# Optimization experiments

Hardware: AMD Instinct MI355X
Metric: run time of the kernel (lower is better)

## Reference

```python
import jax, jax.numpy as jnp
import numpy as np
import math

D_MODEL = 1024
NHEAD = 16
D_K = D_MODEL // NHEAD
B = 4
S = 2048


def setup_inputs() -> dict:
    key = jax.random.key(0)
    ks = jax.random.split(key, 12)
    scale = 1.0 / math.sqrt(D_MODEL)
    inp = {
        "query": jax.random.normal(ks[0], (B, S, D_MODEL), dtype=jnp.float32),
        "key": jax.random.normal(ks[1], (B, S, D_MODEL), dtype=jnp.float32),
        "value": jax.random.normal(ks[2], (B, S, D_MODEL), dtype=jnp.float32),
        "mask": jnp.ones((B, 1, 1, S), dtype=jnp.int32),
        "Wq": jax.random.normal(ks[3], (D_MODEL, D_MODEL), dtype=jnp.float32) * scale,
        "bq": jax.random.normal(ks[4], (D_MODEL,), dtype=jnp.float32) * scale,
        "Wk": jax.random.normal(ks[5], (D_MODEL, D_MODEL), dtype=jnp.float32) * scale,
        "bk": jax.random.normal(ks[6], (D_MODEL,), dtype=jnp.float32) * scale,
        "Wv": jax.random.normal(ks[7], (D_MODEL, D_MODEL), dtype=jnp.float32) * scale,
        "bv": jax.random.normal(ks[8], (D_MODEL,), dtype=jnp.float32) * scale,
        "Wo": jax.random.normal(ks[9], (D_MODEL, D_MODEL), dtype=jnp.float32) * scale,
        "bo": jax.random.normal(ks[10], (D_MODEL,), dtype=jnp.float32) * scale,
    }
    return inp


def reference(query, key, value, mask, Wq, bq, Wk, bk, Wv, bv, Wo, bo):
    b, s, _ = query.shape
    # torch nn.Linear: y = x @ W.T + b ; weights stored [out, in]
    def proj(x, W, bias):
        y = jnp.einsum("bsd,ed->bse", x, W) + bias
        return y.reshape(b, s, NHEAD, D_K).transpose(0, 2, 1, 3)  # [b,h,s,dk]

    Q = proj(query, Wq, bq)
    K = proj(key, Wk, bk)
    V = proj(value, Wv, bv)

    scores = jnp.einsum("bhqd,bhkd->bhqk", Q, K) / math.sqrt(D_K)  # [b,h,s,s]
    scores = jnp.where(mask == 0, jnp.float32(-1e9), scores)
    attn = jax.nn.softmax(scores, axis=-1)
    # dropout p=0.0 (eval): identity
    context = jnp.einsum("bhqk,bhkd->bhqd", attn, V)
    context = context.transpose(0, 2, 1, 3).reshape(b, s, D_MODEL)
    out = jnp.einsum("bsd,ed->bse", context, Wo) + bo
    return out
```

## Files before the change

### kernel.cpp

```cpp
#include <hip/hip_runtime.h>

typedef unsigned short u16;
typedef unsigned int u32;
typedef _Float16 f16;
typedef __attribute__((ext_vector_type(8))) _Float16 f16x8;
typedef __attribute__((ext_vector_type(4))) float f32x4;
typedef __attribute__((ext_vector_type(16))) float f32x16;
typedef __attribute__((ext_vector_type(8))) short short8;
typedef __attribute__((ext_vector_type(4))) short short4v;
typedef __attribute__((ext_vector_type(2))) u32 u32x2;

#define DM 1024
#define NB 4
#define SS 2048
#define NH 16
#define DK 64
#define MROWS (NB * SS)
#define QSCALE 0.1803368801111244f

__device__ __forceinline__ u16 f2h(float x) {
    return __builtin_bit_cast(u16, (f16)x);
}
__device__ __forceinline__ u32 pkh(float lo, float hi) {
    return __builtin_bit_cast(u32, __builtin_amdgcn_cvt_pkrtz(lo, hi));
}

__device__ __forceinline__ f32x4 mfma16h(f16x8 a, f16x8 b, f32x4 c) {
    return __builtin_amdgcn_mfma_f32_16x16x32_f16(a, b, c, 0, 0, 0);
}
__device__ __forceinline__ f32x16 mfma32h(f16x8 a, f16x8 b, f32x16 c) {
    return __builtin_amdgcn_mfma_f32_32x32x16_f16(a, b, c, 0, 0, 0);
}

__device__ __forceinline__ void gload16(const void* g, void* l) {
    __builtin_amdgcn_global_load_lds(
        (const __attribute__((address_space(1))) void*)g,
        (__attribute__((address_space(3))) void*)l, 16, 0, 0);
}

#define PLSWAP(a, b) asm volatile("v_permlane32_swap_b32 %0, %1" : "+v"(a), "+v"(b))


__global__ __launch_bounds__(256) void prep_k(
    const float* __restrict__ q, const float* __restrict__ k, const float* __restrict__ v,
    const float* __restrict__ wq, const float* __restrict__ wk, const float* __restrict__ wv,
    const float* __restrict__ wo,
    u16* __restrict__ xq, u16* __restrict__ xk, u16* __restrict__ xv,
    u16* __restrict__ wqb, u16* __restrict__ wkb, u16* __restrict__ wvb,
    u16* __restrict__ wob) {
    const int NX8 = 1 << 20, NW8 = 1 << 17;
    int i = blockIdx.x * 256 + threadIdx.x;
    const float* src;
    u16* dst;
    int j;
    if (i < 3 * NX8) {
        const int which = i >> 20;
        j = i & (NX8 - 1);
        src = (which == 0) ? q : (which == 1) ? k : v;
        dst = (which == 0) ? xq : (which == 1) ? xk : xv;
    } else {
        const int i2 = i - 3 * NX8;
        const int which = i2 >> 17;
        j = i2 & (NW8 - 1);
        src = (which == 0) ? wq : (which == 1) ? wk : (which == 2) ? wv : wo;
        dst = (which == 0) ? wqb : (which == 1) ? wkb : (which == 2) ? wvb : wob;
    }
    const f32x4* p = (const f32x4*)src + (size_t)j * 2;
    f32x4 a = p[0], b = p[1];
    short8 r;
#pragma unroll
    for (int e = 0; e < 8; e++) r[e] = (short)f2h((e < 4) ? a[e] : b[e - 4]);
    *((short8*)dst + j) = r;
}


__global__ __launch_bounds__(256) void qkv_gemm(
    const u16* __restrict__ Xq, const u16* __restrict__ Xk, const u16* __restrict__ Xv,
    const u16* __restrict__ Wq, const u16* __restrict__ Wk, const u16* __restrict__ Wv,
    const float* __restrict__ bq, const float* __restrict__ bk, const float* __restrict__ bv,
    u16* __restrict__ Qb, u16* __restrict__ Kb, u16* __restrict__ Vb) {
    __shared__ u16 As[128 * 32];
    __shared__ u16 Bs[128 * 32];
    __shared__ u16 Tt[32 * 136];
    const int which = blockIdx.y >> 3;
    const int col0 = (blockIdx.y & 7) * 128;
    const u16* A = (which == 0) ? Xq : (which == 1) ? Xk : Xv;
    const u16* Bw = (which == 0) ? Wq : (which == 1) ? Wk : Wv;
    const float* bias = (which == 0) ? bq : (which == 1) ? bk : bv;
    const float oscale = (which == 0) ? QSCALE : 1.0f;

    const int tid = threadIdx.x;
    const int wid = tid >> 6, lane = tid & 63;
    const int row0 = blockIdx.x * 128;
    const int wr = wid >> 1, wc = wid & 1;
    const int l15 = lane & 15, l4 = lane >> 4;
    const int K = DM;

    f32x4 acc[4][4];
#pragma unroll
    for (int i = 0; i < 4; i++)
#pragma unroll
        for (int j = 0; j < 4; j++) acc[i][j] = f32x4{0.f, 0.f, 0.f, 0.f};

    const int srow = wid * 32 + (lane >> 2);
    const int scol = (lane & 3) * 8;
    const u16* Ag = A + (size_t)(row0 + srow) * K + scol;
    const u16* Bg = Bw + (size_t)(col0 + srow) * K + scol;
    u16* ldsA0 = &As[wid * 1024];
    u16* ldsB0 = &Bs[wid * 1024];

    for (int kt = 0; kt < 32; ++kt) {
        const int ko = kt * 32;
        gload16(Ag + ko, ldsA0);
        gload16(Ag + (size_t)16 * K + ko, ldsA0 + 512);
        gload16(Bg + ko, ldsB0);
        gload16(Bg + (size_t)16 * K + ko, ldsB0 + 512);
        __syncthreads();

        f16x8 af[4], bfr[4];
#pragma unroll
        for (int i = 0; i < 4; i++)
            af[i] = *(const f16x8*)&As[(wr * 64 + i * 16 + l15) * 32 + l4 * 8];
#pragma unroll
        for (int i = 0; i < 4; i++)
            bfr[i] = *(const f16x8*)&Bs[(wc * 64 + i * 16 + l15) * 32 + l4 * 8];
#pragma unroll
        for (int i = 0; i < 4; i++)
#pragma unroll
            for (int j = 0; j < 4; j++) acc[i][j] = mfma16h(af[i], bfr[j], acc[i][j]);
        __syncthreads();
    }

    if (which == 2) {
        const int b = row0 >> 11;
        const int s0 = row0 & (SS - 1);
#pragma unroll
        for (int c = 0; c < 4; ++c) {
            if ((c >> 1) == wc) {
#pragma unroll
                for (int jj = 0; jj < 2; ++jj) {
                    const int j = (c & 1) * 2 + jj;
                    const int col = col0 + wc * 64 + j * 16 + l15;
                    const float bv2 = bias[col];
                    const int dkl = jj * 16 + l15;
#pragma unroll
                    for (int i = 0; i < 4; ++i) {
                        const int sl = wr * 64 + i * 16 + l4 * 4;
                        u32 lo = pkh(acc[i][j][0] + bv2, acc[i][j][1] + bv2);
                        u32 hi2 = pkh(acc[i][j][2] + bv2, acc[i][j][3] + bv2);
                        *(u32x2*)&Tt[dkl * 136 + sl] = u32x2{lo, hi2};
                    }
                }
            }
            __syncthreads();
            {
                const int row = tid >> 3;
                const int col = col0 + c * 32 + row;
                const int h = col >> 6, dk = col & (DK - 1);
                const size_t vbase = ((size_t)(b * NH + h) * DK + dk) * SS + s0;
#pragma unroll
                for (int u = 0; u < 2; ++u) {
                    const int ch = (tid & 7) * 2 + u;
                    f32x4 dat = *(const f32x4*)&Tt[row * 136 + ch * 8];
                    *(f32x4*)&Vb[vbase + ch * 8] = dat;
                }
            }
            __syncthreads();
        }
        return;
    }

    u16* outp = (which == 0) ? Qb : Kb;
#pragma unroll
    for (int j = 0; j < 4; j++) {
        const int col = col0 + wc * 64 + j * 16 + l15;
        const float bv2 = bias[col];
        const int h = col >> 6, dk = col & (DK - 1);
#pragma unroll
        for (int i = 0; i < 4; i++) {
            const int rowb = row0 + wr * 64 + i * 16 + l4 * 4;
#pragma unroll
            for (int r = 0; r < 4; r++) {
                const float v = (acc[i][j][r] + bv2) * oscale;
                const int row = rowb + r;
                const int b = row >> 11, s = row & (SS - 1);
                outp[((size_t)(b * NH + h) * SS + s) * DK + dk] = f2h(v);
            }
        }
    }
}


__global__ __launch_bounds__(256) void out_gemm(const u16* __restrict__ A,
                                                const u16* __restrict__ Bw,
                                                const float* __restrict__ bias,
                                                float* __restrict__ C) {
    __shared__ u16 As[128 * 32];
    __shared__ u16 Bs[128 * 32];
    const int tid = threadIdx.x;
    const int wid = tid >> 6, lane = tid & 63;
    const int row0 = blockIdx.x * 128, col0 = blockIdx.y * 128;
    const int wr = wid >> 1, wc = wid & 1;
    const int l15 = lane & 15, l4 = lane >> 4;
    const int K = DM, N = DM;

    f32x4 acc[4][4];
#pragma unroll
    for (int i = 0; i < 4; i++)
#pragma unroll
        for (int j = 0; j < 4; j++) acc[i][j] = f32x4{0.f, 0.f, 0.f, 0.f};

    const int srow = wid * 32 + (lane >> 2);
    const int scol = (lane & 3) * 8;
    const u16* Ag = A + (size_t)(row0 + srow) * K + scol;
    const u16* Bg = Bw + (size_t)(col0 + srow) * K + scol;
    u16* ldsA0 = &As[wid * 1024];
    u16* ldsB0 = &Bs[wid * 1024];

    for (int kt = 0; kt < 32; ++kt) {
        const int ko = kt * 32;
        gload16(Ag + ko, ldsA0);
        gload16(Ag + (size_t)16 * K + ko, ldsA0 + 512);
        gload16(Bg + ko, ldsB0);
        gload16(Bg + (size_t)16 * K + ko, ldsB0 + 512);
        __syncthreads();

        f16x8 af[4], bfr[4];
#pragma unroll
        for (int i = 0; i < 4; i++)
            af[i] = *(const f16x8*)&As[(wr * 64 + i * 16 + l15) * 32 + l4 * 8];
#pragma unroll
        for (int i = 0; i < 4; i++)
            bfr[i] = *(const f16x8*)&Bs[(wc * 64 + i * 16 + l15) * 32 + l4 * 8];
#pragma unroll
        for (int i = 0; i < 4; i++)
#pragma unroll
            for (int j = 0; j < 4; j++) acc[i][j] = mfma16h(af[i], bfr[j], acc[i][j]);
        __syncthreads();
    }

#pragma unroll
    for (int j = 0; j < 4; j++) {
        const int col = col0 + wc * 64 + j * 16 + l15;
        const float bv = bias[col];
#pragma unroll
        for (int i = 0; i < 4; i++) {
            const int rowb = row0 + wr * 64 + i * 16 + l4 * 4;
#pragma unroll
            for (int r = 0; r < 4; r++)
                C[(size_t)(rowb + r) * N + col] = acc[i][j][r] + bv;
        }
    }
}


__global__ __launch_bounds__(256, 2) void attn6_k(const u16* __restrict__ Q,
                                                  const u16* __restrict__ Kp,
                                                  const u16* __restrict__ Vt,
                                                  u16* __restrict__ ctx) {
    __shared__ u16 Ks[2][4096];
    __shared__ u16 Vs[2][4096];
    const int tid = threadIdx.x, wid = tid >> 6, lane = tid & 63;
    const int l31 = lane & 31, hi = lane >> 5;

    const int flat = blockIdx.y * gridDim.x + blockIdx.x;
    const int xcd = flat & 7, idx = flat >> 3;
    const int bh = xcd * 8 + (idx & 7);
    const int q0 = (idx >> 3) * 256 + wid * 64;

    const size_t base = (size_t)bh * SS * DK;

    f16x8 qf0[4], qf1[4];
#pragma unroll
    for (int dch = 0; dch < 4; dch++) {
        qf0[dch] = *(const f16x8*)&Q[base + (size_t)(q0 + l31) * DK + dch * 16 + hi * 8];
        qf1[dch] = *(const f16x8*)&Q[base + (size_t)(q0 + 32 + l31) * DK + dch * 16 + hi * 8];
    }

    f32x16 acc00, acc01, acc10, acc11;
#pragma unroll
    for (int r = 0; r < 16; r++) { acc00[r] = 0.f; acc01[r] = 0.f; acc10[r] = 0.f; acc11[r] = 0.f; }
    float lrow0 = 0.f, lrow1 = 0.f;

    const int srowA = wid * 16 + (lane >> 3);
    const int srowB = srowA + 8;
    const int scolb = (lane & 7) * 16;
    const int swA = (scolb ^ ((srowA & 7) << 4)) >> 1;
    const int swB = (scolb ^ ((srowB & 7) << 4)) >> 1;
    const u16* KgA = Kp + base + (size_t)srowA * DK + swA;
    const u16* KgB = Kp + base + (size_t)srowB * DK + swB;
    const u16* VgA = Vt + ((size_t)bh * DK + srowA) * SS + swA;
    const u16* VgB = Vt + ((size_t)bh * DK + srowB) * SS + swB;
    const int dstA = wid * 1024, dstB = wid * 1024 + 512;

    gload16(KgA, &Ks[0][dstA]);
    gload16(KgB, &Ks[0][dstB]);
    gload16(VgA, &Vs[0][dstA]);
    gload16(VgB, &Vs[0][dstB]);
    const u16 *KgAn = KgA + 64 * DK, *KgBn = KgB + 64 * DK;
    const u16 *VgAn = VgA + 64, *VgBn = VgB + 64;

    int roff[2][4];
#pragma unroll
    for (int t = 0; t < 2; t++)
#pragma unroll
        for (int c = 0; c < 4; c++)
            roff[t][c] = (t * 32 + l31) * 128 + ((c * 32 + hi * 16) ^ ((l31 & 7) << 4));

#define ATT_BODY(CUR, KT)                                                              \
    {                                                                                  \
        __syncthreads();                                                               \
        if ((KT) + 1 < 32) {                                                           \
            gload16(KgAn, &Ks[(CUR) ^ 1][dstA]);                                       \
            gload16(KgBn, &Ks[(CUR) ^ 1][dstB]);                                       \
            gload16(VgAn, &Vs[(CUR) ^ 1][dstA]);                                       \
            gload16(VgBn, &Vs[(CUR) ^ 1][dstB]);                                       \
            KgAn += 64 * DK; KgBn += 64 * DK;                                          \
            VgAn += 64; VgBn += 64;                                                    \
        }                                                                              \
        const char* kb = (const char*)&Ks[CUR][0];                                     \
        f16x8 kf0[4], kf1[4];                                                          \
        _Pragma("unroll") for (int d = 0; d < 4; d++) {                                \
            kf0[d] = *(const f16x8*)(kb + roff[0][d]);                                 \
            kf1[d] = *(const f16x8*)(kb + roff[1][d]);                                 \
        }                                                                              \
        f32x16 st00 = {}, st01 = {}, st10 = {}, st11 = {};                             \
        __builtin_amdgcn_s_setprio(1);                                                 \
        _Pragma("unroll") for (int d = 0; d < 4; d++) {                                \
            st00 = mfma32h(kf0[d], qf0[d], st00);                                      \
            st01 = mfma32h(kf1[d], qf0[d], st01);                                      \
            st10 = mfma32h(kf0[d], qf1[d], st10);                                      \
            st11 = mfma32h(kf1[d], qf1[d], st11);                                      \
        }                                                                              \
        __builtin_amdgcn_s_setprio(0);                                                 \
        _Pragma("unroll") for (int r = 0; r < 16; r++) {                               \
            st00[r] = __builtin_amdgcn_exp2f(st00[r]);                                 \
            st01[r] = __builtin_amdgcn_exp2f(st01[r]);                                 \
            st10[r] = __builtin_amdgcn_exp2f(st10[r]);                                 \
            st11[r] = __builtin_amdgcn_exp2f(st11[r]);                                 \
        }                                                                              \
        {                                                                              \
            f32x16 t0 = st00 + st01, t1 = st10 + st11;                                 \
            _Pragma("unroll") for (int s2 = 8; s2 >= 1; s2 >>= 1)                      \
                _Pragma("unroll") for (int r = 0; r < s2; r++) {                       \
                    t0[r] += t0[r + s2];                                               \
                    t1[r] += t1[r + s2];                                               \
                }                                                                      \
            lrow0 += t0[0] + __shfl_xor(t0[0], 32);                                    \
            lrow1 += t1[0] + __shfl_xor(t1[0], 32);                                    \
        }                                                                              \
        u32 a0[8], a1[8], b0[8], b1[8];                                                \
        _Pragma("unroll") for (int j = 0; j < 8; j++) {                                \
            a0[j] = pkh(st00[2 * j], st00[2 * j + 1]);                                 \
            a1[j] = pkh(st01[2 * j], st01[2 * j + 1]);                                 \
            b0[j] = pkh(st10[2 * j], st10[2 * j + 1]);                                 \
            b1[j] = pkh(st11[2 * j], st11[2 * j + 1]);                                 \
        }                                                                              \
        PLSWAP(a0[0], a0[2]); PLSWAP(a0[1], a0[3]);                                    \
        PLSWAP(a0[4], a0[6]); PLSWAP(a0[5], a0[7]);                                    \
        PLSWAP(a1[0], a1[2]); PLSWAP(a1[1], a1[3]);                                    \
        PLSWAP(a1[4], a1[6]); PLSWAP(a1[5], a1[7]);                                    \
        PLSWAP(b0[0], b0[2]); PLSWAP(b0[1], b0[3]);                                    \
        PLSWAP(b0[4], b0[6]); PLSWAP(b0[5], b0[7]);                                    \
        PLSWAP(b1[0], b1[2]); PLSWAP(b1[1], b1[3]);                                    \
        PLSWAP(b1[4], b1[6]); PLSWAP(b1[5], b1[7]);                                    \
        union PU { u32 u[4]; f16x8 v; };                                               \
        PU q00, q01, q02, q03, q10, q11, q12, q13;                                     \
        q00.u[0] = a0[0]; q00.u[1] = a0[1]; q00.u[2] = a0[2]; q00.u[3] = a0[3];        \
        q01.u[0] = a0[4]; q01.u[1] = a0[5]; q01.u[2] = a0[6]; q01.u[3] = a0[7];        \
        q02.u[0] = a1[0]; q02.u[1] = a1[1]; q02.u[2] = a1[2]; q02.u[3] = a1[3];        \
        q03.u[0] = a1[4]; q03.u[1] = a1[5]; q03.u[2] = a1[6]; q03.u[3] = a1[7];        \
        q10.u[0] = b0[0]; q10.u[1] = b0[1]; q10.u[2] = b0[2]; q10.u[3] = b0[3];        \
        q11.u[0] = b0[4]; q11.u[1] = b0[5]; q11.u[2] = b0[6]; q11.u[3] = b0[7];        \
        q12.u[0] = b1[0]; q12.u[1] = b1[1]; q12.u[2] = b1[2]; q12.u[3] = b1[3];        \
        q13.u[0] = b1[4]; q13.u[1] = b1[5]; q13.u[2] = b1[6]; q13.u[3] = b1[7];        \
        f16x8 pb0[4] = {q00.v, q01.v, q02.v, q03.v};                                   \
        f16x8 pb1[4] = {q10.v, q11.v, q12.v, q13.v};                                   \
        const char* vb = (const char*)&Vs[CUR][0];                                     \
        f16x8 va0[4], va1[4];                                                          \
        _Pragma("unroll") for (int ks = 0; ks < 4; ks++) {                             \
            va0[ks] = *(const f16x8*)(vb + roff[0][ks]);                               \
            va1[ks] = *(const f16x8*)(vb + roff[1][ks]);                               \
        }                                                                              \
        __builtin_amdgcn_s_setprio(1);                                                 \
        _Pragma("unroll") for (int ks = 0; ks < 4; ks++) {                             \
            acc00 = mfma32h(va0[ks], pb0[ks], acc00);                                  \
            acc01 = mfma32h(va1[ks], pb0[ks], acc01);                                  \
            acc10 = mfma32h(va0[ks], pb1[ks], acc10);                                  \
            acc11 = mfma32h(va1[ks], pb1[ks], acc11);                                  \
        }                                                                              \
        __builtin_amdgcn_s_setprio(0);                                                 \
    }

    for (int kt = 0; kt < 32; kt += 2) {
        ATT_BODY(0, kt);
        ATT_BODY(1, kt + 1);
    }
#undef ATT_BODY

    const int b = bh >> 4, h = bh & (NH - 1);
    const float inv0 = 1.f / lrow0;
    const float inv1 = 1.f / lrow1;
    {
        const int s = q0 + l31;
        const size_t ro = ((size_t)b * SS + s) * DM + h * DK;
#pragma unroll
        for (int g = 0; g < 4; g++) {
            short4v vh;
#pragma unroll
            for (int e = 0; e < 4; e++) vh[e] = (short)f2h(acc00[g * 4 + e] * inv0);
            *(short4v*)&ctx[ro + hi * 4 + g * 8] = vh;
#pragma unroll
            for (int e = 0; e < 4; e++) vh[e] = (short)f2h(acc01[g * 4 + e] * inv0);
            *(short4v*)&ctx[ro + 32 + hi * 4 + g * 8] = vh;
        }
    }
    {
        const int s = q0 + 32 + l31;
        const size_t ro = ((size_t)b * SS + s) * DM + h * DK;
#pragma unroll
        for (int g = 0; g < 4; g++) {
            short4v vh;
#pragma unroll
            for (int e = 0; e < 4; e++) vh[e] = (short)f2h(acc10[g * 4 + e] * inv1);
            *(short4v*)&ctx[ro + hi * 4 + g * 8] = vh;
#pragma unroll
            for (int e = 0; e < 4; e++) vh[e] = (short)f2h(acc11[g * 4 + e] * inv1);
            *(short4v*)&ctx[ro + 32 + hi * 4 + g * 8] = vh;
        }
    }
}


extern "C" void kernel_launch(void* const* d_in, const int* in_sizes, int n_in,
                              void* d_out, int out_size, void* d_ws, size_t ws_size,
                              hipStream_t stream) {
    const float* query = (const float*)d_in[0];
    const float* key   = (const float*)d_in[1];
    const float* value = (const float*)d_in[2];
    const float* Wq = (const float*)d_in[4];
    const float* bq = (const float*)d_in[5];
    const float* Wk = (const float*)d_in[6];
    const float* bk = (const float*)d_in[7];
    const float* Wv = (const float*)d_in[8];
    const float* bv = (const float*)d_in[9];
    const float* Wo = (const float*)d_in[10];
    const float* bo = (const float*)d_in[11];

    const size_t NX = (size_t)MROWS * DM;
    const size_t NW = (size_t)DM * DM;
    const size_t needed = (6 * NX + 4 * NW) * sizeof(u16);
    if (ws_size < needed) return;

    u16* ws = (u16*)d_ws;
    u16* Xq = ws;
    u16* Xk = Xq + NX;
    u16* Xv = Xk + NX;
    u16* Qb = Xv + NX;
    u16* Kb = Qb + NX;
    u16* Vb = Kb + NX;
    u16* Wqb = Vb + NX;
    u16* Wkb = Wqb + NW;
    u16* Wvb = Wkb + NW;
    u16* Wob = Wvb + NW;
    u16* ctx = Xq;

    prep_k<<<14336, 256, 0, stream>>>(query, key, value, Wq, Wk, Wv, Wo,
                                      Xq, Xk, Xv, Wqb, Wkb, Wvb, Wob);

    qkv_gemm<<<dim3(MROWS / 128, 24), 256, 0, stream>>>(Xq, Xk, Xv, Wqb, Wkb, Wvb,
                                                        bq, bk, bv, Qb, Kb, Vb);

    attn6_k<<<dim3(SS / 256, NB * NH), 256, 0, stream>>>(Qb, Kb, Vb, ctx);

    out_gemm<<<dim3(MROWS / 128, DM / 128), 256, 0, stream>>>(ctx, Wob, bo,
                                                              (float*)d_out);
}
```

Before: 207.3 us.

## Remap GEMM blocks across XCDs and stage 128-key tiles per barrier in attention

The QKV and output GEMMs now remap the flat block index so that consecutive row tiles sharing the same weight columns land on the same XCD, aiming for better L2 reuse. The attention kernel now loads two 64-key panels of K and V per stage, which doubles LDS buffers to 64KB. That halves the number of __syncthreads and prefetch issue points per key. The larger LDS footprint may limit occupancy to the two blocks per CU already declared in launch bounds.

```diff
diff --git a/kernel.cpp b/kernel.cpp
--- a/kernel.cpp
+++ b/kernel.cpp
@@ -82,8 +82,14 @@
     __shared__ u16 As[128 * 32];
     __shared__ u16 Bs[128 * 32];
     __shared__ u16 Tt[32 * 136];
-    const int which = blockIdx.y >> 3;
-    const int col0 = (blockIdx.y & 7) * 128;
+
+    const int f = blockIdx.y * gridDim.x + blockIdx.x;
+    const int k8 = f & 7, jj2 = f >> 3;
+    const int bx = k8 * 8 + (jj2 & 7);
+    const int by = jj2 >> 3;
+
+    const int which = by >> 3;
+    const int col0 = (by & 7) * 128;
     const u16* A = (which == 0) ? Xq : (which == 1) ? Xk : Xv;
     const u16* Bw = (which == 0) ? Wq : (which == 1) ? Wk : Wv;
     const float* bias = (which == 0) ? bq : (which == 1) ? bk : bv;
@@ -91,7 +97,7 @@
 
     const int tid = threadIdx.x;
     const int wid = tid >> 6, lane = tid & 63;
-    const int row0 = blockIdx.x * 128;
+    const int row0 = bx * 128;
     const int wr = wid >> 1, wc = wid & 1;
     const int l15 = lane & 15, l4 = lane >> 4;
     const int K = DM;
@@ -138,11 +144,11 @@
         for (int c = 0; c < 4; ++c) {
             if ((c >> 1) == wc) {
 #pragma unroll
-                for (int jj = 0; jj < 2; ++jj) {
-                    const int j = (c & 1) * 2 + jj;
+                for (int jx = 0; jx < 2; ++jx) {
+                    const int j = (c & 1) * 2 + jx;
                     const int col = col0 + wc * 64 + j * 16 + l15;
                     const float bv2 = bias[col];
-                    const int dkl = jj * 16 + l15;
+                    const int dkl = jx * 16 + l15;
 #pragma unroll
                     for (int i = 0; i < 4; ++i) {
                         const int sl = wr * 64 + i * 16 + l4 * 4;
@@ -197,9 +203,15 @@
                                                 float* __restrict__ C) {
     __shared__ u16 As[128 * 32];
     __shared__ u16 Bs[128 * 32];
+
+    const int f = blockIdx.y * gridDim.x + blockIdx.x;
+    const int k8 = f & 7, jj2 = f >> 3;
+    const int bx = k8 * 8 + (jj2 & 7);
+    const int by = jj2 >> 3;
+
     const int tid = threadIdx.x;
     const int wid = tid >> 6, lane = tid & 63;
-    const int row0 = blockIdx.x * 128, col0 = blockIdx.y * 128;
+    const int row0 = bx * 128, col0 = by * 128;
     const int wr = wid >> 1, wc = wid & 1;
     const int l15 = lane & 15, l4 = lane >> 4;
     const int K = DM, N = DM;
@@ -254,12 +266,12 @@
 }
 
 
-__global__ __launch_bounds__(256, 2) void attn6_k(const u16* __restrict__ Q,
+__global__ __launch_bounds__(256, 2) void attn7_k(const u16* __restrict__ Q,
                                                   const u16* __restrict__ Kp,
                                                   const u16* __restrict__ Vt,
                                                   u16* __restrict__ ctx) {
-    __shared__ u16 Ks[2][4096];
-    __shared__ u16 Vs[2][4096];
+    __shared__ u16 Ks[2][2][4096];
+    __shared__ u16 Vs[2][2][4096];
     const int tid = threadIdx.x, wid = tid >> 6, lane = tid & 63;
     const int l31 = lane & 31, hi = lane >> 5;
 
@@ -291,14 +303,25 @@
     const u16* KgB = Kp + base + (size_t)srowB * DK + swB;
     const u16* VgA = Vt + ((size_t)bh * DK + srowA) * SS + swA;
     const u16* VgB = Vt + ((size_t)bh * DK + srowB) * SS + swB;
-    const int dstA = wid * 1024, dstB = wid * 1024 + 512;
-
-    gload16(KgA, &Ks[0][dstA]);
-    gload16(KgB, &Ks[0][dstB]);
-    gload16(VgA, &Vs[0][dstA]);
-    gload16(VgB, &Vs[0][dstB]);
-    const u16 *KgAn = KgA + 64 * DK, *KgBn = KgB + 64 * DK;
-    const u16 *VgAn = VgA + 64, *VgBn = VgB + 64;
+    const int dstA = wid * 512, dstB = wid * 512 + 256;
+
+    const int dA = wid * 1024, dB = wid * 1024 + 512;
+
+#define STAGE(BUF, KT)                                                                 \
+    {                                                                                  \
+        const size_t ko = (size_t)(KT) * 128 * DK;                                     \
+        const size_t vo = (size_t)(KT) * 128;                                          \
+        gload16(KgA + ko, &Ks[BUF][0][dA]);                                            \
+        gload16(KgB + ko, &Ks[BUF][0][dB]);                                            \
+        gload16(KgA + ko + (size_t)64 * DK, &Ks[BUF][1][dA]);                          \
+        gload16(KgB + ko + (size_t)64 * DK, &Ks[BUF][1][dB]);                          \
+        gload16(VgA + vo, &Vs[BUF][0][dA]);                                            \
+        gload16(VgB + vo, &Vs[BUF][0][dB]);                                            \
+        gload16(VgA + vo + 64, &Vs[BUF][1][dA]);                                       \
+        gload16(VgB + vo + 64, &Vs[BUF][1][dB]);                                       \
+    }
+
+    STAGE(0, 0);
 
     int roff[2][4];
 #pragma unroll
@@ -307,18 +330,9 @@
         for (int c = 0; c < 4; c++)
             roff[t][c] = (t * 32 + l31) * 128 + ((c * 32 + hi * 16) ^ ((l31 & 7) << 4));
 
-#define ATT_BODY(CUR, KT)                                                              \
+#define PANEL_BODY(CUR, TH)                                                            \
     {                                                                                  \
-        __syncthreads();                                                               \
-        if ((KT) + 1 < 32) {                                                           \
-            gload16(KgAn, &Ks[(CUR) ^ 1][dstA]);                                       \
-            gload16(KgBn, &Ks[(CUR) ^ 1][dstB]);                                       \
-            gload16(VgAn, &Vs[(CUR) ^ 1][dstA]);                                       \
-            gload16(VgBn, &Vs[(CUR) ^ 1][dstB]);                                       \
-            KgAn += 64 * DK; KgBn += 64 * DK;                                          \
-            VgAn += 64; VgBn += 64;                                                    \
-        }                                                                              \
-        const char* kb = (const char*)&Ks[CUR][0];                                     \
+        const char* kb = (const char*)&Ks[CUR][TH][0];                                 \
         f16x8 kf0[4], kf1[4];                                                          \
         _Pragma("unroll") for (int d = 0; d < 4; d++) {                                \
             kf0[d] = *(const f16x8*)(kb + roff[0][d]);                                 \
@@ -376,7 +390,7 @@
         q13.u[0] = b1[4]; q13.u[1] = b1[5]; q13.u[2] = b1[6]; q13.u[3] = b1[7];        \
         f16x8 pb0[4] = {q00.v, q01.v, q02.v, q03.v};                                   \
         f16x8 pb1[4] = {q10.v, q11.v, q12.v, q13.v};                                   \
-        const char* vb = (const char*)&Vs[CUR][0];                                     \
+        const char* vb = (const char*)&Vs[CUR][TH][0];                                 \
         f16x8 va0[4], va1[4];                                                          \
         _Pragma("unroll") for (int ks = 0; ks < 4; ks++) {                             \
             va0[ks] = *(const f16x8*)(vb + roff[0][ks]);                               \
@@ -392,11 +406,15 @@
         __builtin_amdgcn_s_setprio(0);                                                 \
     }
 
-    for (int kt = 0; kt < 32; kt += 2) {
-        ATT_BODY(0, kt);
-        ATT_BODY(1, kt + 1);
-    }
-#undef ATT_BODY
+    for (int kt = 0; kt < SS / 128; ++kt) {
+        const int cur = kt & 1;
+        __syncthreads();
+        if (kt + 1 < SS / 128) STAGE(cur ^ 1, kt + 1);
+        PANEL_BODY(cur, 0);
+        PANEL_BODY(cur, 1);
+    }
+#undef PANEL_BODY
+#undef STAGE
 
     const int b = bh >> 4, h = bh & (NH - 1);
     const float inv0 = 1.f / lrow0;
@@ -468,11 +486,10 @@
     prep_k<<<14336, 256, 0, stream>>>(query, key, value, Wq, Wk, Wv, Wo,
                                       Xq, Xk, Xv, Wqb, Wkb, Wvb, Wob);
 
-    qkv_gemm<<<dim3(MROWS / 128, 24), 256, 0, stream>>>(Xq, Xk, Xv, Wqb, Wkb, Wvb,
-                                                        bq, bk, bv, Qb, Kb, Vb);
-
-    attn6_k<<<dim3(SS / 256, NB * NH), 256, 0, stream>>>(Qb, Kb, Vb, ctx);
-
-    out_gemm<<<dim3(MROWS / 128, DM / 128), 256, 0, stream>>>(ctx, Wob, bo,
-                                                              (float*)d_out);
-}
+    qkv_gemm<<<dim3(64, 24), 256, 0, stream>>>(Xq, Xk, Xv, Wqb, Wkb, Wvb,
+                                               bq, bk, bv, Qb, Kb, Vb);
+
+    attn7_k<<<dim3(SS / 256, NB * NH), 256, 0, stream>>>(Qb, Kb, Vb, ctx);
+
+    out_gemm<<<dim3(64, 8), 256, 0, stream>>>(ctx, Wob, bo, (float*)d_out);
+}
```

After: 225.7 us. 8.8% more time.
